# Kernel optimization log

Measured on AMD Instinct MI355X. Metric: run time of the kernel, lower is better.

## Reference

```python
import jax, jax.numpy as jnp
import numpy as np

B, S, D, H, F = 2, 1024, 2048, 16, 8192
DH = D // H
MAX_ALPHA = 0.2
CN_SCALE = D / (D - 1)  # CenterNorm scale factor dim/(dim-1)


def setup_inputs() -> dict:
    key = jax.random.key(0)
    ks = jax.random.split(key, 8)
    s = 0.02
    f32 = jnp.float32
    return {
        "x": jax.random.normal(ks[0], (B, S, D), f32),
        "ln1_g": jnp.ones((D,), f32), "ln1_b": jnp.zeros((D,), f32),
        "wq": jax.random.normal(ks[1], (D, D), f32) * s, "bq": jnp.zeros((D,), f32),
        "wk": jax.random.normal(ks[2], (D, D), f32) * s, "bk": jnp.zeros((D,), f32),
        "wv": jax.random.normal(ks[3], (D, D), f32) * s, "bv": jnp.zeros((D,), f32),
        "wo": jax.random.normal(ks[4], (D, D), f32) * s, "bo": jnp.zeros((D,), f32),
        "tau": jnp.ones((H,), f32),   # learnable per-head temperature, init_tau=1.0
        "nu": jnp.ones((H,), f32),    # learnable per-head output scale, init_nu=1.0
        "alpha1": jnp.full((D,), 0.1, f32),  # per-channel residual weight, init 0.1
        "ln2_g": jnp.ones((D,), f32), "ln2_b": jnp.zeros((D,), f32),
        "w1": jax.random.normal(ks[5], (F, D), f32) * s, "b1": jnp.zeros((F,), f32),
        "w2": jax.random.normal(ks[6], (D, F), f32) * s, "b2": jnp.zeros((D,), f32),
        "alpha2": jnp.full((D,), 0.1, f32),
    }


def _center_norm(x, g, b):
    # CenterNorm: subtract mean only (no variance), scale by dim/(dim-1)
    mu = jnp.mean(x, axis=-1, keepdims=True)
    return g * (CN_SCALE * (x - mu)) + b


def _l2norm(t):
    return t / (jnp.linalg.norm(t, axis=-1, keepdims=True) + 1e-6)


def _cosine_attn(x, wq, bq, wk, bk, wv, bv, wo, bo, tau, nu):
    # project and split heads -> [B,H,S,DH]
    def proj(w, b):
        return (jnp.einsum('bsd,ed->bse', x, w) + b).reshape(B, S, H, DH).transpose(0, 2, 1, 3)
    q, k, v = proj(wq, bq), proj(wk, bk), proj(wv, bv)
    qn, kn = _l2norm(q), _l2norm(k)  # cosine similarity attention
    scores = jnp.einsum('bhqd,bhkd->bhqk', qn, kn) * tau[None, :, None, None]
    causal = jnp.tril(jnp.ones((S, S), bool))
    scores = jnp.where(causal[None, None], scores, -jnp.inf)
    p = jax.nn.softmax(scores, axis=-1)
    o = jnp.einsum('bhqk,bhkd->bhqd', p, v) * nu[None, :, None, None]
    o = o.transpose(0, 2, 1, 3).reshape(B, S, D)
    return jnp.einsum('bsd,ed->bse', o, wo) + bo


def _ffn(x, w1, b1, w2, b2):
    h = jax.nn.gelu(jnp.einsum('bsd,fd->bsf', x, w1) + b1)
    return jnp.einsum('bsf,df->bsd', h, w2) + b2


def reference(x, ln1_g, ln1_b, wq, bq, wk, bk, wv, bv, wo, bo, tau, nu,
              alpha1, ln2_g, ln2_b, w1, b1, w2, b2, alpha2):
    a = _center_norm(x, ln1_g, ln1_b)
    a1 = jnp.clip(alpha1, -MAX_ALPHA, MAX_ALPHA)
    x1 = a + a1 * _cosine_attn(a, wq, bq, wk, bk, wv, bv, wo, bo, tau, nu)
    m = _center_norm(x1, ln2_g, ln2_b)
    a2 = jnp.clip(alpha2, -MAX_ALPHA, MAX_ALPHA)
    return m + a2 * _ffn(m, w1, b1, w2, b2)
```

## Files before the change

### kernel.cpp

```cpp
#include <hip/hip_runtime.h>
#include <hip/hip_bf16.h>
#include <stdint.h>

#define B_ 2
#define S_ 1024
#define D_ 2048
#define H_ 16
#define F_ 8192
#define DH_ 128
#define M_ 2048

typedef unsigned short u16;
typedef __attribute__((ext_vector_type(8))) short short8;
typedef __attribute__((ext_vector_type(4))) float f32x4;
typedef __attribute__((ext_vector_type(2))) float f32x2;
typedef __attribute__((ext_vector_type(4))) unsigned short u16x4;

__device__ __forceinline__ u16 f2bf(float f) {
  union { float f; uint32_t u; } c; c.f = f;
  uint32_t r = c.u + 0x7FFFu + ((c.u >> 16) & 1u);
  return (u16)(r >> 16);
}

__device__ __forceinline__ float bf2f(u16 v) {
  union { uint32_t u; float f; } c; c.u = ((uint32_t)v) << 16;
  return c.f;
}

__device__ __forceinline__ void gload16(const void* g, void* l) {
  __builtin_amdgcn_global_load_lds((const __attribute__((address_space(1))) void*)g,
                                   (__attribute__((address_space(3))) void*)l, 16, 0, 0);
}

__device__ __forceinline__ float clipa(float a) {
  return fminf(0.2f, fmaxf(-0.2f, a));
}

__device__ __forceinline__ float gelu_f(float x) {
  float z = 0.7978845608028654f * (x + 0.044715f * x * x * x);
  z = fminf(10.f, fmaxf(-10.f, z));
  float e = __expf(2.f * z);
  return 0.5f * x * (1.f + (e - 1.f) / (e + 1.f));
}

__global__ __launch_bounds__(256) void k_cvt_all(const float* __restrict__ wq,
                                                 const float* __restrict__ wk,
                                                 const float* __restrict__ wv,
                                                 const float* __restrict__ wo,
                                                 const float* __restrict__ w1,
                                                 const float* __restrict__ w2,
                                                 u16* __restrict__ dst) {
  const int t = blockIdx.x * 256 + threadIdx.x;
  const float* srcs[24];
#pragma unroll
  for (int k = 0; k < 8; k++) {
    const float* base = (k < 2) ? wq : (k < 4) ? wk : (k < 6) ? wv : wo;
    srcs[k] = base + (size_t)(k & 1) * 2097152 + (size_t)t * 4;
  }
#pragma unroll
  for (int k = 0; k < 8; k++) srcs[8 + k] = w1 + (size_t)k * 2097152 + (size_t)t * 4;
#pragma unroll
  for (int k = 0; k < 8; k++) srcs[16 + k] = w2 + (size_t)k * 2097152 + (size_t)t * 4;

#pragma unroll
  for (int g = 0; g < 6; g++) {
    f32x4 v[4];
#pragma unroll
    for (int u = 0; u < 4; u++) v[u] = *(const f32x4*)srcs[g * 4 + u];
#pragma unroll
    for (int u = 0; u < 4; u++) {
      u16x4 o;
      o[0] = f2bf(v[u][0]); o[1] = f2bf(v[u][1]);
      o[2] = f2bf(v[u][2]); o[3] = f2bf(v[u][3]);
      *(u16x4*)(dst + ((size_t)(g * 4 + u) * 524288 + t) * 4) = o;
    }
  }
}

__global__ __launch_bounds__(256) void k_centernorm(const float* __restrict__ x,
                                                    const float* __restrict__ g,
                                                    const float* __restrict__ bb,
                                                    float* __restrict__ of,
                                                    u16* __restrict__ ob) {
  const int row = blockIdx.x;
  const int t = threadIdx.x;
  const float* xr = x + (size_t)row * D_;
  f32x4 v0 = *(const f32x4*)(xr + t * 8);
  f32x4 v1 = *(const f32x4*)(xr + t * 8 + 4);
  float s = v0[0] + v0[1] + v0[2] + v0[3] + v1[0] + v1[1] + v1[2] + v1[3];
#pragma unroll
  for (int off = 1; off < 64; off <<= 1) s += __shfl_xor(s, off);
  __shared__ float red[4];
  if ((t & 63) == 0) red[t >> 6] = s;
  __syncthreads();
  const float mu = (red[0] + red[1] + red[2] + red[3]) * (1.0f / D_);
  const float CNS = (float)D_ / (float)(D_ - 1);
  f32x4 g0 = *(const f32x4*)(g + t * 8);
  f32x4 g1 = *(const f32x4*)(g + t * 8 + 4);
  f32x4 b0 = *(const f32x4*)(bb + t * 8);
  f32x4 b1 = *(const f32x4*)(bb + t * 8 + 4);
  f32x4 y0, y1;
  short8 yb;
#pragma unroll
  for (int i = 0; i < 4; i++) {
    y0[i] = g0[i] * (CNS * (v0[i] - mu)) + b0[i];
    y1[i] = g1[i] * (CNS * (v1[i] - mu)) + b1[i];
  }
#pragma unroll
  for (int i = 0; i < 4; i++) { yb[i] = (short)f2bf(y0[i]); yb[4 + i] = (short)f2bf(y1[i]); }
  float* orow = of + (size_t)row * D_;
  *(f32x4*)(orow + t * 8) = y0;
  *(f32x4*)(orow + t * 8 + 4) = y1;
  *(short8*)(ob + (size_t)row * D_ + t * 8) = yb;
}

template <int EPI>
__device__ __forceinline__ void gemm256_core(const u16* __restrict__ A,
                                             const u16* __restrict__ Bt,
                                             const float* __restrict__ bias,
                                             float* __restrict__ outf,
                                             u16* __restrict__ outb,
                                             int N, int K, int kbase, int nk,
                                             int m0, int n0,
                                             const float* __restrict__ tau,
                                             u16* __restrict__ qkv, int z) {
  __shared__ char lds[2][65536];
  const int t = threadIdx.x;
  const int l = t & 63, w = t >> 6;
  const int wr = w >> 2, wc = w & 3;
  const int l15 = l & 15, lhi = l >> 4;
  const int sw = (l15 & 7) << 4;
  const int ab0 = l15 * 128 + ((lhi * 16) ^ sw);
  const int ab1 = l15 * 128 + ((64 + lhi * 16) ^ sw);

  auto stage = [&](int kt, int h) {
#pragma unroll
    for (int rj = 0; rj < 4; rj++) {
      const int region = rj >> 1, j = rj & 1;
      const int pl = h * 16384 + j * 8192 + t * 16;
      const int row = pl >> 7;
      const int scol = (pl & 127) ^ ((row & 7) << 4);
      const int grow = (region ? n0 : m0) + row;
      const char* src = (const char*)(region ? Bt : A) +
                        (size_t)grow * (size_t)(K * 2) +
                        (size_t)((kbase + kt * 64) * 2 + scol);
      gload16(src, &lds[kt & 1][region * 32768 + pl]);
    }
  };

  f32x4 acc[8][4] = {};

  stage(0, 0); stage(0, 1); stage(1, 0);
  asm volatile("s_waitcnt vmcnt(4)" ::: "memory");
  __builtin_amdgcn_s_barrier();
  __builtin_amdgcn_sched_barrier(0);

  for (int kt = 0; kt < nk; ++kt) {
    const char* base = &lds[kt & 1][0];
    const char* pA0 = base + wr * 4096 + ab0;
    const char* pA1 = base + wr * 4096 + ab1;
    const char* pB0 = base + 32768 + wc * 8192 + ab0;
    const char* pB1 = base + 32768 + wc * 8192 + ab1;
    short8 bf[4][2];
#pragma unroll
    for (int ni = 0; ni < 4; ni++) {
      bf[ni][0] = *(const short8*)(pB0 + ni * 2048);
      bf[ni][1] = *(const short8*)(pB1 + ni * 2048);
    }
#pragma unroll
    for (int q = 0; q < 4; q++) {
      short8 aq[2][2];
#pragma unroll
      for (int mi = 0; mi < 2; mi++) {
        aq[mi][0] = *(const short8*)(pA0 + q * 8192 + mi * 2048);
        aq[mi][1] = *(const short8*)(pA1 + q * 8192 + mi * 2048);
      }
      if (q == 1 && kt + 1 < nk) stage(kt + 1, 1);
      if (q == 3 && kt + 2 < nk) stage(kt + 2, 0);
      __builtin_amdgcn_s_setprio(1);
#pragma unroll
      for (int ks = 0; ks < 2; ks++)
#pragma unroll
        for (int mi = 0; mi < 2; mi++)
#pragma unroll
          for (int ni = 0; ni < 4; ni++)
            acc[q * 2 + mi][ni] = __builtin_amdgcn_mfma_f32_16x16x32_bf16(
                aq[mi][ks], bf[ni][ks], acc[q * 2 + mi][ni], 0, 0, 0);
      __builtin_amdgcn_s_setprio(0);
      if (q == 1) __builtin_amdgcn_s_barrier();
    }
    if (kt + 1 < nk) {
      if (kt + 2 < nk) { asm volatile("s_waitcnt vmcnt(4)" ::: "memory"); }
      else             { asm volatile("s_waitcnt vmcnt(0)" ::: "memory"); }
      __builtin_amdgcn_s_barrier();
      __builtin_amdgcn_sched_barrier(0);
    }
  }

  if constexpr (EPI == 4) {
    __shared__ float part[4][256];
#pragma unroll
    for (int ni = 0; ni < 4; ni++) {
      const float bc = bias[n0 + wc * 64 + ni * 16 + l15];
#pragma unroll
      for (int ai = 0; ai < 8; ai++)
#pragma unroll
        for (int j = 0; j < 4; j++) acc[ai][ni][j] += bc;
    }
    if (z < 2) {
      float p[8][4];
#pragma unroll
      for (int ai = 0; ai < 8; ai++)
#pragma unroll
        for (int j = 0; j < 4; j++) {
          p[ai][j] = acc[ai][0][j] * acc[ai][0][j] + acc[ai][1][j] * acc[ai][1][j] +
                     acc[ai][2][j] * acc[ai][2][j] + acc[ai][3][j] * acc[ai][3][j];
#pragma unroll
          for (int off = 1; off < 16; off <<= 1) p[ai][j] += __shfl_xor(p[ai][j], off);
        }
      if (l15 == 0) {
#pragma unroll
        for (int ai = 0; ai < 8; ai++)
#pragma unroll
          for (int j = 0; j < 4; j++) {
            const int rb = (ai >> 1) * 64 + wr * 32 + (ai & 1) * 16 + lhi * 4 + j;
            part[wc][rb] = p[ai][j];
          }
      }
    }
    __syncthreads();
    const int hl = wc >> 1;
    const int hglob = (n0 >> 7) + hl;
    const float tauh = (z == 0) ? tau[hglob] : 1.f;
    char* yt = (char*)&lds[0][0] + w * 16384;
#pragma unroll
    for (int ai = 0; ai < 8; ai++) {
#pragma unroll
      for (int j = 0; j < 4; j++) {
        float sc = 1.f;
        if (z < 2) {
          const int rb = (ai >> 1) * 64 + wr * 32 + (ai & 1) * 16 + lhi * 4 + j;
          const float ssq = part[2 * hl][rb] + part[2 * hl + 1][rb];
          sc = tauh / (sqrtf(ssq) + 1e-6f);
        }
        const int rl = (ai >> 1) * 32 + (ai & 1) * 16 + lhi * 4 + j;
        const int swz = (rl & 7) << 4;
#pragma unroll
        for (int ni = 0; ni < 4; ni++) {
          const int cbyte = (ni * 16 + l15) * 2;
          *(u16*)(yt + rl * 128 + (cbyte ^ swz)) = f2bf(acc[ai][ni][j] * sc);
        }
      }
    }
    __syncthreads();
#pragma unroll
    for (int pass = 0; pass < 16; pass++) {
      const int rl = pass * 8 + (l >> 3);
      const int cb = (l & 7) * 16;
      const short8 v = *(const short8*)(yt + rl * 128 + (cb ^ ((rl & 7) << 4)));
      const int m = m0 + ((rl >> 5) << 6) + wr * 32 + (rl & 31);
      const int bb2 = m >> 10, s = m & 1023;
      const int d = (wc & 1) * 64 + (cb >> 1);
      *(short8*)(qkv + (((size_t)(bb2 * H_ + hglob)) * S_ + s) * DH_ + d) = v;
    }
    return;
  }

#pragma unroll
  for (int ni = 0; ni < 4; ni++) {
    const int col = n0 + wc * 64 + ni * 16 + l15;
    const float bcol = (EPI == 3) ? 0.f : bias[col];
#pragma unroll
    for (int ai = 0; ai < 8; ai++) {
      const int row = m0 + (ai >> 1) * 64 + wr * 32 + (ai & 1) * 16 + lhi * 4;
#pragma unroll
      for (int j = 0; j < 4; j++) {
        const float v = acc[ai][ni][j] + bcol;
        const size_t idx = (size_t)(row + j) * N + col;
        if (EPI == 0) outf[idx] = v;
        else if (EPI == 2) outb[idx] = f2bf(gelu_f(v));
        else outb[idx] = f2bf(v);
      }
    }
  }
}

__global__ __launch_bounds__(512, 2) void k_qkv256(const u16* A, const u16* W,
                                                   const float* b0, const float* b1,
                                                   const float* b2, const float* tau,
                                                   u16* qn, u16* kn, u16* vn) {
  const int z = blockIdx.z;
  const u16* Bt = W + (size_t)z * 4194304;
  const float* bias = z == 0 ? b0 : (z == 1 ? b1 : b2);
  u16* dst = z == 0 ? qn : (z == 1 ? kn : vn);
  gemm256_core<4>(A, Bt, bias, nullptr, nullptr, D_, D_, 0, 32,
                  blockIdx.y * 256, blockIdx.x * 256, tau, dst, z);
}

__global__ __launch_bounds__(512, 2) void k_ffn1_256(const u16* A, const u16* Bt,
                                                     const float* bias, u16* outb) {
  gemm256_core<2>(A, Bt, bias, nullptr, outb, F_, D_, 0, 32,
                  blockIdx.y * 256, blockIdx.x * 256, nullptr, nullptr, 0);
}

__global__ __launch_bounds__(512, 2) void k_ffn2_256(const u16* A, const u16* Bt, u16* P) {
  gemm256_core<3>(A, Bt, nullptr, nullptr, P + (size_t)blockIdx.z * M_ * D_, D_, F_,
                  blockIdx.z * 2048, 32, blockIdx.y * 256, blockIdx.x * 256,
                  nullptr, nullptr, 0);
}

__global__ __launch_bounds__(256, 2) void k_oproj(const u16* __restrict__ A,
                                                  const u16* __restrict__ Bt,
                                                  const float* __restrict__ bias,
                                                  const float* __restrict__ res,
                                                  const float* __restrict__ alpha,
                                                  float* __restrict__ outf) {
  const int N = D_, K = D_, nk = 32;
  const int m0 = blockIdx.y * 128, n0 = blockIdx.x * 128;
  __shared__ char lds[2][32768];
  const int t = threadIdx.x;
  const int l = t & 63, w = t >> 6;
  const int wr = w >> 1, wc = w & 1;
  const int l15 = l & 15, lhi = l >> 4;
  const int sw = (l15 & 7) << 4;
  const int ab0 = l15 * 128 + ((lhi * 16) ^ sw);
  const int ab1 = l15 * 128 + ((64 + lhi * 16) ^ sw);

  auto stage = [&](int kt, int h) {
#pragma unroll
    for (int rj = 0; rj < 4; rj++) {
      const int region = rj >> 1, j = rj & 1;
      const int pl = h * 8192 + j * 4096 + t * 16;
      const int row = pl >> 7;
      const int scol = (pl & 127) ^ ((row & 7) << 4);
      const int grow = (region ? n0 : m0) + row;
      const char* src = (const char*)(region ? Bt : A) +
                        (size_t)grow * (size_t)(K * 2) + (size_t)(kt * 128 + scol);
      gload16(src, &lds[kt & 1][region * 16384 + pl]);
    }
  };

  f32x4 acc[4][4] = {};
  stage(0, 0); stage(0, 1); stage(1, 0);
  asm volatile("s_waitcnt vmcnt(4)" ::: "memory");
  __builtin_amdgcn_s_barrier();
  __builtin_amdgcn_sched_barrier(0);

  for (int kt = 0; kt < nk; ++kt) {
    const char* base = &lds[kt & 1][0];
    const char* pB0 = base + 16384 + wc * 8192 + ab0;
    const char* pB1 = base + 16384 + wc * 8192 + ab1;
    short8 bf[4][2];
#pragma unroll
    for (int ni = 0; ni < 4; ni++) {
      bf[ni][0] = *(const short8*)(pB0 + ni * 2048);
      bf[ni][1] = *(const short8*)(pB1 + ni * 2048);
    }
#pragma unroll
    for (int q = 0; q < 2; q++) {
      short8 aq[2][2];
#pragma unroll
      for (int mi = 0; mi < 2; mi++) {
        aq[mi][0] = *(const short8*)(base + q * 8192 + wr * 4096 + mi * 2048 + ab0);
        aq[mi][1] = *(const short8*)(base + q * 8192 + wr * 4096 + mi * 2048 + ab1);
      }
      if (q == 0 && kt + 1 < nk) stage(kt + 1, 1);
      if (q == 1 && kt + 2 < nk) stage(kt + 2, 0);
      __builtin_amdgcn_s_setprio(1);
#pragma unroll
      for (int ks = 0; ks < 2; ks++)
#pragma unroll
        for (int mi = 0; mi < 2; mi++)
#pragma unroll
          for (int ni = 0; ni < 4; ni++)
            acc[q * 2 + mi][ni] = __builtin_amdgcn_mfma_f32_16x16x32_bf16(
                aq[mi][ks], bf[ni][ks], acc[q * 2 + mi][ni], 0, 0, 0);
      __builtin_amdgcn_s_setprio(0);
      if (q == 0) __builtin_amdgcn_s_barrier();
    }
    if (kt + 1 < nk) {
      if (kt + 2 < nk) { asm volatile("s_waitcnt vmcnt(4)" ::: "memory"); }
      else             { asm volatile("s_waitcnt vmcnt(0)" ::: "memory"); }
      __builtin_amdgcn_s_barrier();
      __builtin_amdgcn_sched_barrier(0);
    }
  }

#pragma unroll
  for (int ni = 0; ni < 4; ni++) {
    const int col = n0 + wc * 64 + ni * 16 + l15;
    const float bcol = bias[col];
    const float alc = clipa(alpha[col]);
#pragma unroll
    for (int ai = 0; ai < 4; ai++) {
      const int row = m0 + (ai >> 1) * 64 + wr * 32 + (ai & 1) * 16 + lhi * 4;
#pragma unroll
      for (int j = 0; j < 4; j++) {
        const size_t idx = (size_t)(row + j) * N + col;
        outf[idx] = res[idx] + alc * (acc[ai][ni][j] + bcol);
      }
    }
  }
}

__global__ __launch_bounds__(256) void k_ffn2_combine(const u16* __restrict__ P,
                                                      const float* __restrict__ bias,
                                                      const float* __restrict__ res,
                                                      const float* __restrict__ alpha,
                                                      float* __restrict__ out) {
  const int i = blockIdx.x * 256 + threadIdx.x;
  const size_t base = (size_t)i * 8;
  const int col = (int)(base & (D_ - 1));
  const size_t PS = (size_t)M_ * D_;
  float s[8] = {};
#pragma unroll
  for (int p = 0; p < 4; p++) {
    short8 v = *(const short8*)(P + p * PS + base);
#pragma unroll
    for (int j = 0; j < 8; j++) s[j] += bf2f((u16)v[j]);
  }
  f32x4 b0 = *(const f32x4*)(bias + col);
  f32x4 b1 = *(const f32x4*)(bias + col + 4);
  f32x4 a0 = *(const f32x4*)(alpha + col);
  f32x4 a1 = *(const f32x4*)(alpha + col + 4);
  f32x4 r0 = *(const f32x4*)(res + base);
  f32x4 r1 = *(const f32x4*)(res + base + 4);
  f32x4 o0, o1;
#pragma unroll
  for (int j = 0; j < 4; j++) {
    o0[j] = r0[j] + clipa(a0[j]) * (s[j] + b0[j]);
    o1[j] = r1[j] + clipa(a1[j]) * (s[4 + j] + b1[j]);
  }
  *(f32x4*)(out + base) = o0;
  *(f32x4*)(out + base + 4) = o1;
}

__global__ __launch_bounds__(256) void k_attn(const u16* __restrict__ qn,
                                              const u16* __restrict__ kn,
                                              const u16* __restrict__ vn,
                                              const float* __restrict__ nu,
                                              u16* __restrict__ o) {
  __shared__ u16 Ks[64 * 128];
  __shared__ u16 Vt[128 * 64];
  __shared__ u16 Pl[4][16][72];
  const int t = threadIdx.x;
  const int l = t & 63, w = t >> 6;
  const int l15 = l & 15, lhi = l >> 4;
  const int qt = blockIdx.x;
  const int bh = blockIdx.y;
  const int h = bh & (H_ - 1);
  const int b = bh >> 4;
  const size_t hoff = (size_t)bh * S_ * DH_;
  const u16* Qh = qn + hoff;
  const u16* Kh = kn + hoff;
  const u16* Vh = vn + hoff;
  const int q0 = qt * 64;
  const int r0 = q0 + w * 16;
  short8 qf[4];
#pragma unroll
  for (int kk = 0; kk < 4; kk++)
    qf[kk] = *(const short8*)(Qh + (size_t)(r0 + l15) * DH_ + kk * 32 + lhi * 8);
  float mrow[4], lrow[4];
  f32x4 oacc[8] = {};
#pragma unroll
  for (int j = 0; j < 4; j++) { mrow[j] = -1e30f; lrow[j] = 0.f; }

  for (int kv0 = 0; kv0 < q0 + 64; kv0 += 64) {
#pragma unroll
    for (int i = 0; i < 4; i++) {
      const int p = i * 4096 + t * 16;
      const int row = p >> 8;
      const int colb = p & 255;
      const int scolb = colb ^ ((row & 7) << 4);
      gload16((const char*)(Kh + (size_t)(kv0 + row) * DH_) + scolb, (char*)Ks + p);
    }
#pragma unroll
    for (int i = 0; i < 4; i++) {
      const int c0 = w * 8 + i * 32;
      const int r = l;
      short8 vv = *(const short8*)(Vh + (size_t)(kv0 + r) * DH_ + c0);
#pragma unroll
      for (int j = 0; j < 8; j++) {
        const int ba = ((c0 + j) * 128 + r * 2) ^ (((c0 + j) & 7) << 4);
        *(u16*)((char*)Vt + ba) = (u16)vv[j];
      }
    }
    __syncthreads();
    f32x4 st[4] = {};
#pragma unroll
    for (int ks = 0; ks < 4; ks++) {
#pragma unroll
      for (int ct = 0; ct < 4; ct++) {
        const int n = ct * 16 + l15;
        const int ka = (ks * 32 + lhi * 8) * 2;
        short8 kf = *(const short8*)((const char*)Ks + n * 256 + (ka ^ ((n & 7) << 4)));
        st[ct] = __builtin_amdgcn_mfma_f32_16x16x32_bf16(qf[ks], kf, st[ct], 0, 0, 0);
      }
    }
    float pm[4] = {-1e30f, -1e30f, -1e30f, -1e30f};
#pragma unroll
    for (int ct = 0; ct < 4; ct++) {
      const int col = kv0 + ct * 16 + l15;
#pragma unroll
      for (int j = 0; j < 4; j++) {
        const int row = r0 + lhi * 4 + j;
        float s = st[ct][j];
        s = (col <= row) ? s : -1e30f;
        st[ct][j] = s;
        pm[j] = fmaxf(pm[j], s);
      }
    }
#pragma unroll
    for (int j = 0; j < 4; j++) {
#pragma unroll
      for (int off = 1; off < 16; off <<= 1) pm[j] = fmaxf(pm[j], __shfl_xor(pm[j], off));
    }
    float scl[4], psum[4];
#pragma unroll
    for (int j = 0; j < 4; j++) {
      const float nm = fmaxf(mrow[j], pm[j]);
      scl[j] = __expf(mrow[j] - nm);
      mrow[j] = nm;
      psum[j] = 0.f;
    }
#pragma unroll
    for (int ct = 0; ct < 4; ct++) {
#pragma unroll
      for (int j = 0; j < 4; j++) {
        const float p = __expf(st[ct][j] - mrow[j]);
        psum[j] += p;
        Pl[w][lhi * 4 + j][ct * 16 + l15] = f2bf(p);
      }
    }
#pragma unroll
    for (int j = 0; j < 4; j++) {
#pragma unroll
      for (int off = 1; off < 16; off <<= 1) psum[j] += __shfl_xor(psum[j], off);
      lrow[j] = lrow[j] * scl[j] + psum[j];
    }
#pragma unroll
    for (int nt = 0; nt < 8; nt++) {
#pragma unroll
      for (int j = 0; j < 4; j++) oacc[nt][j] *= scl[j];
    }
#pragma unroll
    for (int ks2 = 0; ks2 < 2; ks2++) {
      short8 pa = *(const short8*)((const char*)&Pl[w][0][0] + l15 * 144 + ks2 * 64 + lhi * 16);
#pragma unroll
      for (int nt = 0; nt < 8; nt++) {
        const int n = nt * 16 + l15;
        const int ba = (n * 128 + (ks2 * 32 + lhi * 8) * 2) ^ ((n & 7) << 4);
        short8 vf = *(const short8*)((const char*)Vt + ba);
        oacc[nt] = __builtin_amdgcn_mfma_f32_16x16x32_bf16(pa, vf, oacc[nt], 0, 0, 0);
      }
    }
    __syncthreads();
  }
  const float num = nu[h];
  float rs[4];
#pragma unroll
  for (int j = 0; j < 4; j++) rs[j] = num / lrow[j];
#pragma unroll
  for (int nt = 0; nt < 8; nt++) {
    const int col = h * DH_ + nt * 16 + l15;
#pragma unroll
    for (int j = 0; j < 4; j++) {
      const int row = r0 + lhi * 4 + j;
      o[((size_t)b * S_ + row) * D_ + col] = f2bf(oacc[nt][j] * rs[j]);
    }
  }
}

extern "C" void kernel_launch(void* const* d_in, const int* in_sizes, int n_in,
                              void* d_out, int out_size, void* d_ws, size_t ws_size,
                              hipStream_t stream) {
  const float* x    = (const float*)d_in[0];
  const float* ln1g = (const float*)d_in[1];
  const float* ln1b = (const float*)d_in[2];
  const float* wq   = (const float*)d_in[3];
  const float* bq   = (const float*)d_in[4];
  const float* wk   = (const float*)d_in[5];
  const float* bk   = (const float*)d_in[6];
  const float* wv   = (const float*)d_in[7];
  const float* bv   = (const float*)d_in[8];
  const float* wo   = (const float*)d_in[9];
  const float* bo   = (const float*)d_in[10];
  const float* tau  = (const float*)d_in[11];
  const float* nu   = (const float*)d_in[12];
  const float* al1  = (const float*)d_in[13];
  const float* ln2g = (const float*)d_in[14];
  const float* ln2b = (const float*)d_in[15];
  const float* w1   = (const float*)d_in[16];
  const float* b1   = (const float*)d_in[17];
  const float* w2   = (const float*)d_in[18];
  const float* b2   = (const float*)d_in[19];
  const float* al2  = (const float*)d_in[20];

  char* ws = (char*)d_ws;
  u16* WQ = (u16*)(ws + 0);
  u16* WO = (u16*)(ws + 25165824);
  u16* W1B = (u16*)(ws + 33554432);
  u16* W2B = (u16*)(ws + 67108864);
  float* AF = (float*)(ws + 100663296);
  u16*   AB = (u16*)(ws + 117440512);
  u16*   OB = (u16*)(ws + 125829120);
  u16*   MB = (u16*)(ws + 134217728);
  float* X1 = (float*)(ws + 142606336);
  float* MF2 = (float*)(ws + 159383552);
  u16* QN = (u16*)(ws + 176160768);
  u16* KN = (u16*)(ws + 184549376);
  u16* VN = (u16*)(ws + 192937984);
  u16*   HB = (u16*)(ws + 176160768);
  u16*   P4 = (u16*)(ws + 0);

  k_cvt_all<<<2048, 256, 0, stream>>>(wq, wk, wv, wo, w1, w2, WQ);

  k_centernorm<<<M_, 256, 0, stream>>>(x, ln1g, ln1b, AF, AB);

  k_qkv256<<<dim3(8, 8, 3), 512, 0, stream>>>(AB, WQ, bq, bk, bv, tau, QN, KN, VN);

  k_attn<<<dim3(S_ / 64, B_ * H_), 256, 0, stream>>>(QN, KN, VN, nu, OB);

  k_oproj<<<dim3(16, 16), 256, 0, stream>>>(OB, WO, bo, AF, al1, X1);

  k_centernorm<<<M_, 256, 0, stream>>>(X1, ln2g, ln2b, MF2, MB);

  k_ffn1_256<<<dim3(32, 8), 512, 0, stream>>>(MB, W1B, b1, HB);

  k_ffn2_256<<<dim3(8, 8, 4), 512, 0, stream>>>(HB, W2B, P4);
  k_ffn2_combine<<<2048, 256, 0, stream>>>(P4, b2, MF2, al2, (float*)d_out);
}
```

Baseline: 390.5 us.

## Fuse fp32-to-bf16 weight conversion into GEMM B-tile staging

Drops the separate pass that converts every weight matrix to bf16 up front. Each GEMM now loads fp32 weight tiles into registers, converts them to bf16, and writes them to LDS itself. This avoids a full read and write of about 100MB of weights, but each weight tile is now re-read as fp32 by every M-block. The pipeline also shrinks from a two-tile-ahead async prefetch to a one-tile register-staged prefetch with full waits each iteration, which may expose more latency.

```diff
diff --git a/kernel.cpp b/kernel.cpp
--- a/kernel.cpp
+++ b/kernel.cpp
@@ -13,8 +13,6 @@
 typedef unsigned short u16;
 typedef __attribute__((ext_vector_type(8))) short short8;
 typedef __attribute__((ext_vector_type(4))) float f32x4;
-typedef __attribute__((ext_vector_type(2))) float f32x2;
-typedef __attribute__((ext_vector_type(4))) unsigned short u16x4;
 
 __device__ __forceinline__ u16 f2bf(float f) {
   union { float f; uint32_t u; } c; c.f = f;
@@ -41,40 +39,6 @@
   z = fminf(10.f, fmaxf(-10.f, z));
   float e = __expf(2.f * z);
   return 0.5f * x * (1.f + (e - 1.f) / (e + 1.f));
-}
-
-__global__ __launch_bounds__(256) void k_cvt_all(const float* __restrict__ wq,
-                                                 const float* __restrict__ wk,
-                                                 const float* __restrict__ wv,
-                                                 const float* __restrict__ wo,
-                                                 const float* __restrict__ w1,
-                                                 const float* __restrict__ w2,
-                                                 u16* __restrict__ dst) {
-  const int t = blockIdx.x * 256 + threadIdx.x;
-  const float* srcs[24];
-#pragma unroll
-  for (int k = 0; k < 8; k++) {
-    const float* base = (k < 2) ? wq : (k < 4) ? wk : (k < 6) ? wv : wo;
-    srcs[k] = base + (size_t)(k & 1) * 2097152 + (size_t)t * 4;
-  }
-#pragma unroll
-  for (int k = 0; k < 8; k++) srcs[8 + k] = w1 + (size_t)k * 2097152 + (size_t)t * 4;
-#pragma unroll
-  for (int k = 0; k < 8; k++) srcs[16 + k] = w2 + (size_t)k * 2097152 + (size_t)t * 4;
-
-#pragma unroll
-  for (int g = 0; g < 6; g++) {
-    f32x4 v[4];
-#pragma unroll
-    for (int u = 0; u < 4; u++) v[u] = *(const f32x4*)srcs[g * 4 + u];
-#pragma unroll
-    for (int u = 0; u < 4; u++) {
-      u16x4 o;
-      o[0] = f2bf(v[u][0]); o[1] = f2bf(v[u][1]);
-      o[2] = f2bf(v[u][2]); o[3] = f2bf(v[u][3]);
-      *(u16x4*)(dst + ((size_t)(g * 4 + u) * 524288 + t) * 4) = o;
-    }
-  }
 }
 
 __global__ __launch_bounds__(256) void k_centernorm(const float* __restrict__ x,
@@ -115,10 +79,9 @@
 }
 
 template <int EPI>
-__device__ __forceinline__ void gemm256_core(const u16* __restrict__ A,
-                                             const u16* __restrict__ Bt,
+__device__ __forceinline__ void gemm256_f32b(const u16* __restrict__ A,
+                                             const float* __restrict__ Bt32,
                                              const float* __restrict__ bias,
-                                             float* __restrict__ outf,
                                              u16* __restrict__ outb,
                                              int N, int K, int kbase, int nk,
                                              int m0, int n0,
@@ -133,25 +96,52 @@
   const int ab0 = l15 * 128 + ((lhi * 16) ^ sw);
   const int ab1 = l15 * 128 + ((64 + lhi * 16) ^ sw);
 
-  auto stage = [&](int kt, int h) {
-#pragma unroll
-    for (int rj = 0; rj < 4; rj++) {
-      const int region = rj >> 1, j = rj & 1;
+  auto stage_a = [&](int kt, int h) {
+#pragma unroll
+    for (int j = 0; j < 2; j++) {
       const int pl = h * 16384 + j * 8192 + t * 16;
       const int row = pl >> 7;
       const int scol = (pl & 127) ^ ((row & 7) << 4);
-      const int grow = (region ? n0 : m0) + row;
-      const char* src = (const char*)(region ? Bt : A) +
-                        (size_t)grow * (size_t)(K * 2) +
+      const char* src = (const char*)A + (size_t)(m0 + row) * (size_t)(K * 2) +
                         (size_t)((kbase + kt * 64) * 2 + scol);
-      gload16(src, &lds[kt & 1][region * 32768 + pl]);
+      gload16(src, &lds[kt & 1][pl]);
     }
   };
 
+  f32x4 bld[8];
+  auto stage_b_load = [&](int kt) {
+#pragma unroll
+    for (int s = 0; s < 4; s++) {
+      const int pl = s * 8192 + t * 16;
+      const int row = pl >> 7;
+      const int scol = (pl & 127) ^ ((row & 7) << 4);
+      const float* src = Bt32 + (size_t)(n0 + row) * (size_t)K +
+                         (size_t)(kbase + kt * 64 + (scol >> 1));
+      bld[s * 2 + 0] = *(const f32x4*)(src);
+      bld[s * 2 + 1] = *(const f32x4*)(src + 4);
+    }
+  };
+  auto stage_b_write = [&](int kt) {
+#pragma unroll
+    for (int s = 0; s < 4; s++) {
+      const int pl = s * 8192 + t * 16;
+      short8 o;
+#pragma unroll
+      for (int e = 0; e < 4; e++) {
+        o[e] = (short)f2bf(bld[s * 2][e]);
+        o[4 + e] = (short)f2bf(bld[s * 2 + 1][e]);
+      }
+      *(short8*)(&lds[kt & 1][32768 + pl]) = o;
+    }
+  };
+
   f32x4 acc[8][4] = {};
 
-  stage(0, 0); stage(0, 1); stage(1, 0);
-  asm volatile("s_waitcnt vmcnt(4)" ::: "memory");
+  stage_b_load(0);
+  stage_a(0, 0); stage_a(0, 1);
+  stage_b_write(0);
+  asm volatile("s_waitcnt vmcnt(0)" ::: "memory");
+  asm volatile("s_waitcnt lgkmcnt(0)" ::: "memory");
   __builtin_amdgcn_s_barrier();
   __builtin_amdgcn_sched_barrier(0);
 
@@ -161,6 +151,7 @@
     const char* pA1 = base + wr * 4096 + ab1;
     const char* pB0 = base + 32768 + wc * 8192 + ab0;
     const char* pB1 = base + 32768 + wc * 8192 + ab1;
+    const bool more = (kt + 1 < nk);
     short8 bf[4][2];
 #pragma unroll
     for (int ni = 0; ni < 4; ni++) {
@@ -175,8 +166,12 @@
         aq[mi][0] = *(const short8*)(pA0 + q * 8192 + mi * 2048);
         aq[mi][1] = *(const short8*)(pA1 + q * 8192 + mi * 2048);
       }
-      if (q == 1 && kt + 1 < nk) stage(kt + 1, 1);
-      if (q == 3 && kt + 2 < nk) stage(kt + 2, 0);
+      if (q == 1 && more) {
+        stage_b_load(kt + 1);
+        stage_a(kt + 1, 0);
+        stage_a(kt + 1, 1);
+      }
+      if (q == 3 && more) stage_b_write(kt + 1);
       __builtin_amdgcn_s_setprio(1);
 #pragma unroll
       for (int ks = 0; ks < 2; ks++)
@@ -189,9 +184,9 @@
       __builtin_amdgcn_s_setprio(0);
       if (q == 1) __builtin_amdgcn_s_barrier();
     }
-    if (kt + 1 < nk) {
-      if (kt + 2 < nk) { asm volatile("s_waitcnt vmcnt(4)" ::: "memory"); }
-      else             { asm volatile("s_waitcnt vmcnt(0)" ::: "memory"); }
+    if (more) {
+      asm volatile("s_waitcnt lgkmcnt(0)" ::: "memory");
+      asm volatile("s_waitcnt vmcnt(0)" ::: "memory");
       __builtin_amdgcn_s_barrier();
       __builtin_amdgcn_sched_barrier(0);
     }
@@ -277,40 +272,40 @@
       for (int j = 0; j < 4; j++) {
         const float v = acc[ai][ni][j] + bcol;
         const size_t idx = (size_t)(row + j) * N + col;
-        if (EPI == 0) outf[idx] = v;
-        else if (EPI == 2) outb[idx] = f2bf(gelu_f(v));
+        if (EPI == 2) outb[idx] = f2bf(gelu_f(v));
         else outb[idx] = f2bf(v);
       }
     }
   }
 }
 
-__global__ __launch_bounds__(512, 2) void k_qkv256(const u16* A, const u16* W,
+__global__ __launch_bounds__(512, 2) void k_qkv256(const u16* A, const float* wq,
+                                                   const float* wk, const float* wv,
                                                    const float* b0, const float* b1,
                                                    const float* b2, const float* tau,
                                                    u16* qn, u16* kn, u16* vn) {
   const int z = blockIdx.z;
-  const u16* Bt = W + (size_t)z * 4194304;
+  const float* Bt = z == 0 ? wq : (z == 1 ? wk : wv);
   const float* bias = z == 0 ? b0 : (z == 1 ? b1 : b2);
   u16* dst = z == 0 ? qn : (z == 1 ? kn : vn);
-  gemm256_core<4>(A, Bt, bias, nullptr, nullptr, D_, D_, 0, 32,
+  gemm256_f32b<4>(A, Bt, bias, nullptr, D_, D_, 0, 32,
                   blockIdx.y * 256, blockIdx.x * 256, tau, dst, z);
 }
 
-__global__ __launch_bounds__(512, 2) void k_ffn1_256(const u16* A, const u16* Bt,
+__global__ __launch_bounds__(512, 2) void k_ffn1_256(const u16* A, const float* w1,
                                                      const float* bias, u16* outb) {
-  gemm256_core<2>(A, Bt, bias, nullptr, outb, F_, D_, 0, 32,
+  gemm256_f32b<2>(A, w1, bias, outb, F_, D_, 0, 32,
                   blockIdx.y * 256, blockIdx.x * 256, nullptr, nullptr, 0);
 }
 
-__global__ __launch_bounds__(512, 2) void k_ffn2_256(const u16* A, const u16* Bt, u16* P) {
-  gemm256_core<3>(A, Bt, nullptr, nullptr, P + (size_t)blockIdx.z * M_ * D_, D_, F_,
+__global__ __launch_bounds__(512, 2) void k_ffn2_256(const u16* A, const float* w2, u16* P) {
+  gemm256_f32b<3>(A, w2, nullptr, P + (size_t)blockIdx.z * M_ * D_, D_, F_,
                   blockIdx.z * 2048, 32, blockIdx.y * 256, blockIdx.x * 256,
                   nullptr, nullptr, 0);
 }
 
 __global__ __launch_bounds__(256, 2) void k_oproj(const u16* __restrict__ A,
-                                                  const u16* __restrict__ Bt,
+                                                  const float* __restrict__ Bt32,
                                                   const float* __restrict__ bias,
                                                   const float* __restrict__ res,
                                                   const float* __restrict__ alpha,
@@ -326,23 +321,51 @@
   const int ab0 = l15 * 128 + ((lhi * 16) ^ sw);
   const int ab1 = l15 * 128 + ((64 + lhi * 16) ^ sw);
 
-  auto stage = [&](int kt, int h) {
-#pragma unroll
-    for (int rj = 0; rj < 4; rj++) {
-      const int region = rj >> 1, j = rj & 1;
+  auto stage_a = [&](int kt, int h) {
+#pragma unroll
+    for (int j = 0; j < 2; j++) {
       const int pl = h * 8192 + j * 4096 + t * 16;
       const int row = pl >> 7;
       const int scol = (pl & 127) ^ ((row & 7) << 4);
-      const int grow = (region ? n0 : m0) + row;
-      const char* src = (const char*)(region ? Bt : A) +
-                        (size_t)grow * (size_t)(K * 2) + (size_t)(kt * 128 + scol);
-      gload16(src, &lds[kt & 1][region * 16384 + pl]);
+      const char* src = (const char*)A + (size_t)(m0 + row) * (size_t)(K * 2) +
+                        (size_t)(kt * 128 + scol);
+      gload16(src, &lds[kt & 1][pl]);
     }
   };
 
+  f32x4 bld[8];
+  auto stage_b_load = [&](int kt) {
+#pragma unroll
+    for (int s = 0; s < 4; s++) {
+      const int pl = s * 4096 + t * 16;
+      const int row = pl >> 7;
+      const int scol = (pl & 127) ^ ((row & 7) << 4);
+      const float* src = Bt32 + (size_t)(n0 + row) * (size_t)K +
+                         (size_t)(kt * 64 + (scol >> 1));
+      bld[s * 2 + 0] = *(const f32x4*)(src);
+      bld[s * 2 + 1] = *(const f32x4*)(src + 4);
+    }
+  };
+  auto stage_b_write = [&](int kt) {
+#pragma unroll
+    for (int s = 0; s < 4; s++) {
+      const int pl = s * 4096 + t * 16;
+      short8 o;
+#pragma unroll
+      for (int e = 0; e < 4; e++) {
+        o[e] = (short)f2bf(bld[s * 2][e]);
+        o[4 + e] = (short)f2bf(bld[s * 2 + 1][e]);
+      }
+      *(short8*)(&lds[kt & 1][16384 + pl]) = o;
+    }
+  };
+
   f32x4 acc[4][4] = {};
-  stage(0, 0); stage(0, 1); stage(1, 0);
-  asm volatile("s_waitcnt vmcnt(4)" ::: "memory");
+  stage_b_load(0);
+  stage_a(0, 0); stage_a(0, 1);
+  stage_b_write(0);
+  asm volatile("s_waitcnt vmcnt(0)" ::: "memory");
+  asm volatile("s_waitcnt lgkmcnt(0)" ::: "memory");
   __builtin_amdgcn_s_barrier();
   __builtin_amdgcn_sched_barrier(0);
 
@@ -350,6 +373,7 @@
     const char* base = &lds[kt & 1][0];
     const char* pB0 = base + 16384 + wc * 8192 + ab0;
     const char* pB1 = base + 16384 + wc * 8192 + ab1;
+    const bool more = (kt + 1 < nk);
     short8 bf[4][2];
 #pragma unroll
     for (int ni = 0; ni < 4; ni++) {
@@ -364,8 +388,12 @@
         aq[mi][0] = *(const short8*)(base + q * 8192 + wr * 4096 + mi * 2048 + ab0);
         aq[mi][1] = *(const short8*)(base + q * 8192 + wr * 4096 + mi * 2048 + ab1);
       }
-      if (q == 0 && kt + 1 < nk) stage(kt + 1, 1);
-      if (q == 1 && kt + 2 < nk) stage(kt + 2, 0);
+      if (q == 0 && more) {
+        stage_b_load(kt + 1);
+        stage_a(kt + 1, 0);
+        stage_a(kt + 1, 1);
+      }
+      if (q == 1 && more) stage_b_write(kt + 1);
       __builtin_amdgcn_s_setprio(1);
 #pragma unroll
       for (int ks = 0; ks < 2; ks++)
@@ -378,9 +406,9 @@
       __builtin_amdgcn_s_setprio(0);
       if (q == 0) __builtin_amdgcn_s_barrier();
     }
-    if (kt + 1 < nk) {
-      if (kt + 2 < nk) { asm volatile("s_waitcnt vmcnt(4)" ::: "memory"); }
-      else             { asm volatile("s_waitcnt vmcnt(0)" ::: "memory"); }
+    if (more) {
+      asm volatile("s_waitcnt lgkmcnt(0)" ::: "memory");
+      asm volatile("s_waitcnt vmcnt(0)" ::: "memory");
       __builtin_amdgcn_s_barrier();
       __builtin_amdgcn_sched_barrier(0);
     }
@@ -597,10 +625,8 @@
   const float* al2  = (const float*)d_in[20];
 
   char* ws = (char*)d_ws;
-  u16* WQ = (u16*)(ws + 0);
-  u16* WO = (u16*)(ws + 25165824);
-  u16* W1B = (u16*)(ws + 33554432);
-  u16* W2B = (u16*)(ws + 67108864);
+  u16*   P4 = (u16*)(ws + 0);
+  u16*   HB = (u16*)(ws + 33554432);
   float* AF = (float*)(ws + 100663296);
   u16*   AB = (u16*)(ws + 117440512);
   u16*   OB = (u16*)(ws + 125829120);
@@ -610,23 +636,19 @@
   u16* QN = (u16*)(ws + 176160768);
   u16* KN = (u16*)(ws + 184549376);
   u16* VN = (u16*)(ws + 192937984);
-  u16*   HB = (u16*)(ws + 176160768);
-  u16*   P4 = (u16*)(ws + 0);
-
-  k_cvt_all<<<2048, 256, 0, stream>>>(wq, wk, wv, wo, w1, w2, WQ);
 
   k_centernorm<<<M_, 256, 0, stream>>>(x, ln1g, ln1b, AF, AB);
 
-  k_qkv256<<<dim3(8, 8, 3), 512, 0, stream>>>(AB, WQ, bq, bk, bv, tau, QN, KN, VN);
+  k_qkv256<<<dim3(8, 8, 3), 512, 0, stream>>>(AB, wq, wk, wv, bq, bk, bv, tau, QN, KN, VN);
 
   k_attn<<<dim3(S_ / 64, B_ * H_), 256, 0, stream>>>(QN, KN, VN, nu, OB);
 
-  k_oproj<<<dim3(16, 16), 256, 0, stream>>>(OB, WO, bo, AF, al1, X1);
+  k_oproj<<<dim3(16, 16), 256, 0, stream>>>(OB, wo, bo, AF, al1, X1);
 
   k_centernorm<<<M_, 256, 0, stream>>>(X1, ln2g, ln2b, MF2, MB);
 
-  k_ffn1_256<<<dim3(32, 8), 512, 0, stream>>>(MB, W1B, b1, HB);
-
-  k_ffn2_256<<<dim3(8, 8, 4), 512, 0, stream>>>(HB, W2B, P4);
+  k_ffn1_256<<<dim3(32, 8), 512, 0, stream>>>(MB, w1, b1, HB);
+
+  k_ffn2_256<<<dim3(8, 8, 4), 512, 0, stream>>>(HB, w2, P4);
   k_ffn2_combine<<<2048, 256, 0, stream>>>(P4, b2, MF2, al2, (float*)d_out);
 }
```

Result: slower. 425.9 us (+9.1%).
